# Kernel tuning notes

Measured on AMD Instinct MI355X. Metric: run time of the kernel, lower is better.

The kernel has to match this reference:

```python
import jax, jax.numpy as jnp
import numpy as np

NUM_HEADS = 8

def _ln(x, w, b, eps=1e-5):
    m = x.mean(-1, keepdims=True)
    v = ((x - m) ** 2).mean(-1, keepdims=True)
    return (x - m) / jnp.sqrt(v + eps) * w + b

def _l2n(x, axis=-1, eps=1e-12):
    n = jnp.linalg.norm(x, axis=axis, keepdims=True)
    return x / jnp.maximum(n, eps)

def setup_inputs() -> dict:
    key = jax.random.key(0)
    ks = jax.random.split(key, 30)
    B, N, C, nc, t = 2, 4096, 256, 150, 3
    Hh = Ww = 64
    hid = 4 * C
    s = 0.02
    inp = {}
    inp['x'] = jax.random.normal(ks[0], (B, N, C), jnp.float32)
    inp['z'] = jax.random.normal(ks[1], (B, nc, (t + 1) * N), jnp.float32)
    inp['mem'] = jax.random.normal(ks[2], (B * t, N, C), jnp.float32)
    inp['clustering_w'] = s * jax.random.normal(ks[3], (nc, C), jnp.float32)
    inp['prompt1'] = jax.random.normal(ks[4], (nc,), jnp.float32)
    inp['tdt1'] = jnp.eye(nc, dtype=jnp.float32) + s * jax.random.normal(ks[5], (nc, nc), jnp.float32)
    inp['prompt2'] = jax.random.normal(ks[6], (nc,), jnp.float32)
    inp['tdt2'] = jnp.eye(nc, dtype=jnp.float32) + s * jax.random.normal(ks[7], (nc, nc), jnp.float32)
    inp['sim_alpha'] = jnp.ones((1,), jnp.float32)
    inp['sim_beta'] = jnp.zeros((1,), jnp.float32)
    inp['q_w'] = s * jax.random.normal(ks[8], (C, C), jnp.float32)
    inp['q_b'] = s * jax.random.normal(ks[9], (C,), jnp.float32)
    inp['k_w'] = s * jax.random.normal(ks[10], (C, C), jnp.float32)
    inp['k_b'] = s * jax.random.normal(ks[11], (C,), jnp.float32)
    inp['v_w'] = s * jax.random.normal(ks[12], (C, C), jnp.float32)
    inp['v_b'] = s * jax.random.normal(ks[13], (C,), jnp.float32)
    inp['proj_w'] = s * jax.random.normal(ks[14], (C, C), jnp.float32)
    inp['proj_b'] = s * jax.random.normal(ks[15], (C,), jnp.float32)
    inp['norm_w'] = jnp.ones((C,), jnp.float32)
    inp['norm_b'] = jnp.zeros((C,), jnp.float32)
    inp['fc1_w'] = s * jax.random.normal(ks[16], (hid, C), jnp.float32)
    inp['fc1_b'] = s * jax.random.normal(ks[17], (hid,), jnp.float32)
    inp['dw_w'] = s * jax.random.normal(ks[18], (hid, 1, 3, 3), jnp.float32)
    inp['dw_b'] = s * jax.random.normal(ks[19], (hid,), jnp.float32)
    inp['fc2_w'] = s * jax.random.normal(ks[20], (C, hid), jnp.float32)
    inp['fc2_b'] = s * jax.random.normal(ks[21], (C,), jnp.float32)
    inp['H'] = Hh
    inp['W'] = Ww
    inp['t'] = t
    return inp

def _forward(x, z, mem, clustering_w, prompt1, tdt1, prompt2, tdt2, sim_alpha, sim_beta,
             q_w, q_b, k_w, k_b, v_w, v_b, proj_w, proj_b, norm_w, norm_b,
             fc1_w, fc1_b, dw_w, dw_b, fc2_w, fc2_b, H, W, t):
    B, N, C = x.shape
    nc = clustering_w.shape[0]
    res = x
    T = t + 1
    # cat memory frames with current frame: [(B*T), N, C]
    xf = jnp.concatenate([mem.reshape(B, t, N, C), x[:, None]], axis=1).reshape(B * T, N, C)
    # clustering head: (SRPS approximated as identity) 1x1 conv dim->num_clusters
    cl = jnp.einsum('bnc,kc->bkn', xf, clustering_w)            # [(B*T), nc, N]
    cl = cl.reshape(B, T, nc, N).transpose(0, 2, 1, 3).reshape(B, nc, T * N)
    # top-down prompt modulation of z and cluster logits
    zc = z.transpose(0, 2, 1)                                   # [B, T*N, nc]
    cos = _l2n(zc, -1) @ _l2n(prompt1[None, :, None], axis=1)   # [B, T*N, 1]
    zc = (zc * jnp.clip(cos, 0.0, 1.0)) @ tdt1
    clc = cl.transpose(0, 2, 1)
    cos = _l2n(clc, -1) @ _l2n(prompt2[None, :, None], axis=1)
    clc = (clc * jnp.clip(cos, 0.0, 1.0)) @ tdt2
    cluster_x_z = ((clc + zc) * 0.5).transpose(0, 2, 1)          # [B, nc, T*N]
    # inner_center: per-frame soft assignment -> cluster centers
    center = cluster_x_z.reshape(B, nc, T, N).transpose(0, 2, 1, 3)  # [B, T, nc, N]
    assigned_results = center
    soft = jax.nn.softmax(center, axis=-1)
    cx = xf.reshape(B, T, N, C)
    cen = jnp.einsum('btkn,btnc->btkc', soft, cx)               # [B, T, nc, C]
    last, prev = cen[:, -1], cen[:, :-1]                        # [B,nc,C], [B,t,nc,C]
    dot = jnp.einsum('bkc,btkc->btk', last, prev)
    denom = jnp.maximum(jnp.linalg.norm(last, axis=-1)[:, None] * jnp.linalg.norm(prev, axis=-1), 1e-8)
    gate = jax.nn.sigmoid(sim_beta + sim_alpha * (dot / denom))  # [B, t, nc]
    C_in = last + (gate[..., None] * prev).sum(axis=1)          # [B, nc, C]
    C_in = _ln(C_in, norm_w, norm_b)
    # cross attention: tokens query cluster centers
    hd = C // NUM_HEADS
    q = (res @ q_w.T + q_b) * (1.0 / np.sqrt(hd))
    k = C_in @ k_w.T + k_b
    v = C_in @ v_w.T + v_b
    q = q.reshape(B, N, NUM_HEADS, hd).transpose(0, 2, 1, 3)
    k = k.reshape(B, nc, NUM_HEADS, hd).transpose(0, 2, 1, 3)
    v = v.reshape(B, nc, NUM_HEADS, hd).transpose(0, 2, 1, 3)
    attn = jax.nn.softmax(jnp.einsum('bhnd,bhkd->bhnk', q, k), axis=-1)
    o = jnp.einsum('bhnk,bhkd->bhnd', attn, v).transpose(0, 2, 1, 3).reshape(B, N, C)
    o = o @ proj_w.T + proj_b
    out = res + _ln(o, norm_w, norm_b)
    # MLP with depthwise conv
    h = out @ fc1_w.T + fc1_b                                   # [B, N, 4C]
    hid = h.shape[-1]
    h_img = h.transpose(0, 2, 1).reshape(B, hid, H, W)
    h_img = jax.lax.conv_general_dilated(h_img, dw_w, (1, 1), 'SAME',
                                         feature_group_count=hid,
                                         dimension_numbers=('NCHW', 'OIHW', 'NCHW'))
    h_img = h_img + dw_b[None, :, None, None]
    h = h_img.reshape(B, hid, N).transpose(0, 2, 1)
    h = jax.nn.gelu(h, approximate=False) @ fc2_w.T + fc2_b
    out = out + _ln(h, norm_w, norm_b)
    return out, cluster_x_z, assigned_results

def reference(x, z, mem, clustering_w, prompt1, tdt1, prompt2, tdt2, sim_alpha, sim_beta,
              q_w, q_b, k_w, k_b, v_w, v_b, proj_w, proj_b, norm_w, norm_b,
              fc1_w, fc1_b, dw_w, dw_b, fc2_w, fc2_b, H, W, t):
    return _forward(x, z, mem, clustering_w, prompt1, tdt1, prompt2, tdt2, sim_alpha, sim_beta,
                    q_w, q_b, k_w, k_b, v_w, v_b, proj_w, proj_b, norm_w, norm_b,
                    fc1_w, fc1_b, dw_w, dw_b, fc2_w, fc2_b, H, W, t)
```

## Files before the change

kernel.cpp:

```cpp
#include <hip/hip_runtime.h>
#include <math.h>


typedef __attribute__((ext_vector_type(8))) short bf16x8;
typedef __attribute__((ext_vector_type(4))) float f32x4;

__device__ __forceinline__ short f2b(float f) {
  union { float f; unsigned int u; } c; c.f = f;
  unsigned int r = (c.u + 0x7fffu + ((c.u >> 16) & 1u)) >> 16;
  return (short)r;
}

__device__ __forceinline__ float bred_sum(float v, float* red) {
  int tid = threadIdx.x;
  red[tid] = v; __syncthreads();
  #pragma unroll
  for (int s = 128; s > 0; s >>= 1) {
    if (tid < s) red[tid] += red[tid + s];
    __syncthreads();
  }
  float r = red[0]; __syncthreads();
  return r;
}

__global__ __launch_bounds__(256) void gemm_mfma(
    const float* __restrict__ A, const float* __restrict__ W,
    const float* __restrict__ bias, float* __restrict__ out,
    int M, int N, int K, float alpha)
{
  __shared__ __align__(16) short As[64 * 72];
  __shared__ __align__(16) short Bs[64 * 72];
  const int tid = threadIdx.x;
  const int m0 = blockIdx.x * 64;
  const int n0 = blockIdx.y * 64;
  const int wave = tid >> 6;
  const int lane = tid & 63;
  const int wm = wave & 1, wn = wave >> 1;
  const int t16 = lane & 15;
  const int k8 = (lane >> 4) * 8;

  f32x4 acc[2][2];
  #pragma unroll
  for (int i = 0; i < 2; ++i)
    #pragma unroll
    for (int j = 0; j < 2; ++j)
      acc[i][j] = (f32x4){0.f, 0.f, 0.f, 0.f};

  const int sr = tid >> 2;
  const int sk = (tid & 3) * 16;

  for (int k0 = 0; k0 < K; k0 += 64) {
    {
      const float* ap = &A[(size_t)(m0 + sr) * K + k0 + sk];
      float4 v0 = *(const float4*)&ap[0];
      float4 v1 = *(const float4*)&ap[4];
      float4 v2 = *(const float4*)&ap[8];
      float4 v3 = *(const float4*)&ap[12];
      bf16x8 w0, w1;
      w0[0] = f2b(v0.x); w0[1] = f2b(v0.y); w0[2] = f2b(v0.z); w0[3] = f2b(v0.w);
      w0[4] = f2b(v1.x); w0[5] = f2b(v1.y); w0[6] = f2b(v1.z); w0[7] = f2b(v1.w);
      w1[0] = f2b(v2.x); w1[1] = f2b(v2.y); w1[2] = f2b(v2.z); w1[3] = f2b(v2.w);
      w1[4] = f2b(v3.x); w1[5] = f2b(v3.y); w1[6] = f2b(v3.z); w1[7] = f2b(v3.w);
      *(bf16x8*)&As[sr * 72 + sk] = w0;
      *(bf16x8*)&As[sr * 72 + sk + 8] = w1;
    }
    {
      const float* wp = &W[(size_t)(n0 + sr) * K + k0 + sk];
      float4 v0 = *(const float4*)&wp[0];
      float4 v1 = *(const float4*)&wp[4];
      float4 v2 = *(const float4*)&wp[8];
      float4 v3 = *(const float4*)&wp[12];
      bf16x8 w0, w1;
      w0[0] = f2b(v0.x); w0[1] = f2b(v0.y); w0[2] = f2b(v0.z); w0[3] = f2b(v0.w);
      w0[4] = f2b(v1.x); w0[5] = f2b(v1.y); w0[6] = f2b(v1.z); w0[7] = f2b(v1.w);
      w1[0] = f2b(v2.x); w1[1] = f2b(v2.y); w1[2] = f2b(v2.z); w1[3] = f2b(v2.w);
      w1[4] = f2b(v3.x); w1[5] = f2b(v3.y); w1[6] = f2b(v3.z); w1[7] = f2b(v3.w);
      *(bf16x8*)&Bs[sr * 72 + sk] = w0;
      *(bf16x8*)&Bs[sr * 72 + sk + 8] = w1;
    }
    __syncthreads();
    #pragma unroll
    for (int ks = 0; ks < 2; ++ks) {
      const int kofs = ks * 32 + k8;
      bf16x8 af0 = *(const bf16x8*)&As[(wm * 32 +  0 + t16) * 72 + kofs];
      bf16x8 af1 = *(const bf16x8*)&As[(wm * 32 + 16 + t16) * 72 + kofs];
      bf16x8 bf0 = *(const bf16x8*)&Bs[(wn * 32 +  0 + t16) * 72 + kofs];
      bf16x8 bf1 = *(const bf16x8*)&Bs[(wn * 32 + 16 + t16) * 72 + kofs];
      acc[0][0] = __builtin_amdgcn_mfma_f32_16x16x32_bf16(af0, bf0, acc[0][0], 0, 0, 0);
      acc[1][0] = __builtin_amdgcn_mfma_f32_16x16x32_bf16(af1, bf0, acc[1][0], 0, 0, 0);
      acc[0][1] = __builtin_amdgcn_mfma_f32_16x16x32_bf16(af0, bf1, acc[0][1], 0, 0, 0);
      acc[1][1] = __builtin_amdgcn_mfma_f32_16x16x32_bf16(af1, bf1, acc[1][1], 0, 0, 0);
    }
    __syncthreads();
  }
  const int r4 = (lane >> 4) * 4;
  #pragma unroll
  for (int ni = 0; ni < 2; ++ni) {
    const int gcol = n0 + wn * 32 + ni * 16 + t16;
    const float bb = bias[gcol];
    #pragma unroll
    for (int mi = 0; mi < 2; ++mi) {
      #pragma unroll
      for (int r = 0; r < 4; ++r) {
        const int gm = m0 + wm * 32 + mi * 16 + r4 + r;
        out[(size_t)gm * N + gcol] = alpha * (acc[mi][ni][r] + bb);
      }
    }
  }
}

__global__ __launch_bounds__(256) void prep_bt(
    const float* __restrict__ cw, const float* __restrict__ tdt2, const float* __restrict__ tdt1,
    short* __restrict__ cwb, short* __restrict__ TT)
{
  int idx = blockIdx.x * 256 + threadIdx.x;
  if (idx < 160 * 256) {
    int kc = idx >> 8, k = idx & 255;
    float v = (kc < 150) ? cw[kc * 256 + k] : 0.f;
    cwb[idx] = f2b(v);
  }
  if (idx < 160 * 320) {
    int kc = idx / 320, kk = idx - kc * 320;
    float t = 0.f;
    if (kc < 150) {
      if (kk < 150) t = tdt2[kk * 150 + kc];
      else if (kk >= 160 && kk < 310) t = tdt1[(kk - 160) * 150 + kc];
    }
    TT[idx] = f2b(t);
  }
}

__global__ __launch_bounds__(256) void xf_t(
    const float* __restrict__ x, const float* __restrict__ mem, short* __restrict__ xfT)
{
  __shared__ float tile[64][257];
  const int bt = blockIdx.y;
  const int n0 = blockIdx.x * 64;
  const int b = bt >> 2, ti = bt & 3;
  const float* xf = (ti < 3) ? (mem + (size_t)(b * 3 + ti) * 4096 * 256)
                             : (x + (size_t)b * 4096 * 256);
  const int tid = threadIdx.x;
  const int r = tid >> 2, cofs = (tid & 3) * 64;
  const float* src = xf + (size_t)(n0 + r) * 256 + cofs;
  #pragma unroll
  for (int i = 0; i < 16; ++i) {
    float4 v = *(const float4*)&src[i * 4];
    tile[r][cofs + i * 4 + 0] = v.x;
    tile[r][cofs + i * 4 + 1] = v.y;
    tile[r][cofs + i * 4 + 2] = v.z;
    tile[r][cofs + i * 4 + 3] = v.w;
  }
  __syncthreads();
  short* dst = xfT + ((size_t)bt * 256 + tid) * 4096 + n0;
  #pragma unroll
  for (int seg = 0; seg < 8; ++seg) {
    bf16x8 w;
    #pragma unroll
    for (int j = 0; j < 8; ++j) w[j] = f2b(tile[seg * 8 + j][tid]);
    *(bf16x8*)&dst[seg * 8] = w;
  }
}

__global__ __launch_bounds__(256) void fused_csz(
    const float* __restrict__ x, const float* __restrict__ mem, const float* __restrict__ z,
    const short* __restrict__ cwb, const short* __restrict__ TT,
    const float* __restrict__ p1, const float* __restrict__ p2,
    float* __restrict__ csz, float* __restrict__ asg)
{
  __shared__ __align__(16) short Acatile[64 * 328];
  __shared__ float p1s[160], p2s[160];
  __shared__ float sred[4][16][9];
  __shared__ float czs[64];
  const int tid = threadIdx.x;
  const int r0 = blockIdx.x * 64;
  const int b = r0 >> 14;
  const int mmg = r0 & 16383;
  const int ti = mmg >> 12, nn = mmg & 4095;
  const float* Ab = ((ti < 3) ? (mem + (size_t)(b * 3 + ti) * 4096 * 256)
                              : (x + (size_t)b * 4096 * 256)) + (size_t)nn * 256;
  const int wave = tid >> 6, lane = tid & 63;
  const int t16 = lane & 15, quad = lane >> 4, k8 = quad * 8;

  const int kr = tid >> 4, c4 = (tid & 15) * 4;
  float4 zv[10];
  #pragma unroll
  for (int it = 0; it < 10; ++it) {
    const int k = it * 16 + kr;
    zv[it] = make_float4(0.f, 0.f, 0.f, 0.f);
    if (k < 150) zv[it] = *(const float4*)&z[((size_t)b * 150 + k) * 16384 + mmg + c4];
  }
  if (tid < 160) {
    p2s[tid] = (tid < 150) ? p2[tid] : 0.f;
    p1s[tid] = (tid < 150) ? p1[tid] : 0.f;
  }

  f32x4 acc[10];
  #pragma unroll
  for (int i = 0; i < 10; ++i) acc[i] = (f32x4){0.f, 0.f, 0.f, 0.f};
  {
    const float* ap = Ab + (size_t)(wave * 16 + t16) * 256 + k8;
    const short* bp = cwb + t16 * 256 + k8;
    #pragma unroll 2
    for (int ks = 0; ks < 8; ++ks) {
      float4 v0 = *(const float4*)&ap[ks * 32];
      float4 v1 = *(const float4*)&ap[ks * 32 + 4];
      bf16x8 a;
      a[0] = f2b(v0.x); a[1] = f2b(v0.y); a[2] = f2b(v0.z); a[3] = f2b(v0.w);
      a[4] = f2b(v1.x); a[5] = f2b(v1.y); a[6] = f2b(v1.z); a[7] = f2b(v1.w);
      #pragma unroll
      for (int nf = 0; nf < 10; ++nf) {
        bf16x8 bv = *(const bf16x8*)&bp[nf * 4096 + ks * 32];
        acc[nf] = __builtin_amdgcn_mfma_f32_16x16x32_bf16(a, bv, acc[nf], 0, 0, 0);
      }
    }
  }
  __syncthreads();

  {
    float d[4] = {0.f, 0.f, 0.f, 0.f}, s[4] = {0.f, 0.f, 0.f, 0.f};
    float pn = 0.f;
    #pragma unroll
    for (int nf = 0; nf < 10; ++nf) {
      float a2 = p2s[nf * 16 + t16];
      pn += a2 * a2;
      #pragma unroll
      for (int r = 0; r < 4; ++r) {
        float v = acc[nf][r];
        d[r] = fmaf(v, a2, d[r]);
        s[r] = fmaf(v, v, s[r]);
      }
    }
    #pragma unroll
    for (int off = 1; off < 16; off <<= 1) {
      pn += __shfl_xor(pn, off);
      #pragma unroll
      for (int r = 0; r < 4; ++r) {
        d[r] += __shfl_xor(d[r], off);
        s[r] += __shfl_xor(s[r], off);
      }
    }
    const float spn = fmaxf(sqrtf(pn), 1e-12f);
    float cs[4];
    #pragma unroll
    for (int r = 0; r < 4; ++r) {
      float c = d[r] / (fmaxf(sqrtf(s[r]), 1e-12f) * spn);
      cs[r] = fminf(fmaxf(c, 0.f), 1.f);
    }
    #pragma unroll
    for (int nf = 0; nf < 10; ++nf)
      #pragma unroll
      for (int r = 0; r < 4; ++r)
        Acatile[(wave * 16 + quad * 4 + r) * 328 + nf * 16 + t16] = f2b(acc[nf][r] * cs[r]);
  }

  {
    float d[4] = {0.f, 0.f, 0.f, 0.f}, sv[4] = {0.f, 0.f, 0.f, 0.f};
    float pn = 0.f;
    #pragma unroll
    for (int it = 0; it < 10; ++it) {
      const int k = it * 16 + kr;
      const float a = p1s[k];
      d[0] = fmaf(zv[it].x, a, d[0]); d[1] = fmaf(zv[it].y, a, d[1]);
      d[2] = fmaf(zv[it].z, a, d[2]); d[3] = fmaf(zv[it].w, a, d[3]);
      sv[0] = fmaf(zv[it].x, zv[it].x, sv[0]); sv[1] = fmaf(zv[it].y, zv[it].y, sv[1]);
      sv[2] = fmaf(zv[it].z, zv[it].z, sv[2]); sv[3] = fmaf(zv[it].w, zv[it].w, sv[3]);
      pn = fmaf(a, a, pn);
    }
    #pragma unroll
    for (int off = 16; off < 64; off <<= 1) {
      pn += __shfl_xor(pn, off);
      #pragma unroll
      for (int r = 0; r < 4; ++r) {
        d[r] += __shfl_xor(d[r], off);
        sv[r] += __shfl_xor(sv[r], off);
      }
    }
    if ((lane >> 4) == 0) {
      #pragma unroll
      for (int r = 0; r < 4; ++r) {
        sred[wave][lane][r] = d[r];
        sred[wave][lane][4 + r] = sv[r];
      }
      sred[wave][lane][8] = pn;
    }
  }
  __syncthreads();
  if (tid < 64) {
    const int cg = tid >> 2, r = tid & 3;
    float dd = 0.f, ss = 0.f, pp = 0.f;
    #pragma unroll
    for (int w = 0; w < 4; ++w) {
      dd += sred[w][cg][r];
      ss += sred[w][cg][4 + r];
      pp += sred[w][cg][8];
    }
    float c = dd / (fmaxf(sqrtf(ss), 1e-12f) * fmaxf(sqrtf(pp), 1e-12f));
    czs[tid] = fminf(fmaxf(c, 0.f), 1.f);
  }
  __syncthreads();
  {
    const float cz0 = czs[c4 + 0], cz1 = czs[c4 + 1], cz2 = czs[c4 + 2], cz3 = czs[c4 + 3];
    #pragma unroll
    for (int it = 0; it < 10; ++it) {
      const int k = it * 16 + kr;
      Acatile[(c4 + 0) * 328 + 160 + k] = f2b(zv[it].x * cz0);
      Acatile[(c4 + 1) * 328 + 160 + k] = f2b(zv[it].y * cz1);
      Acatile[(c4 + 2) * 328 + 160 + k] = f2b(zv[it].z * cz2);
      Acatile[(c4 + 3) * 328 + 160 + k] = f2b(zv[it].w * cz3);
    }
  }
  __syncthreads();

  {
    const int wm = wave & 1, wn = wave >> 1;
    f32x4 c2[2][5];
    #pragma unroll
    for (int i = 0; i < 2; ++i)
      #pragma unroll
      for (int j = 0; j < 5; ++j)
        c2[i][j] = (f32x4){0.f, 0.f, 0.f, 0.f};
    const short* bp = TT + (size_t)(wn * 80 + t16) * 320 + k8;
    #pragma unroll 2
    for (int ks = 0; ks < 10; ++ks) {
      bf16x8 a0 = *(const bf16x8*)&Acatile[(wm * 32 + t16) * 328 + ks * 32 + k8];
      bf16x8 a1 = *(const bf16x8*)&Acatile[(wm * 32 + 16 + t16) * 328 + ks * 32 + k8];
      #pragma unroll
      for (int nf = 0; nf < 5; ++nf) {
        bf16x8 bv = *(const bf16x8*)&bp[nf * 5120 + ks * 32];
        c2[0][nf] = __builtin_amdgcn_mfma_f32_16x16x32_bf16(a0, bv, c2[0][nf], 0, 0, 0);
        c2[1][nf] = __builtin_amdgcn_mfma_f32_16x16x32_bf16(a1, bv, c2[1][nf], 0, 0, 0);
      }
    }
    #pragma unroll
    for (int nf = 0; nf < 5; ++nf) {
      const int kc = wn * 80 + nf * 16 + t16;
      if (kc < 150) {
        #pragma unroll
        for (int mf = 0; mf < 2; ++mf) {
          const int moff = wm * 32 + mf * 16 + quad * 4;
          float4 r4;
          r4.x = 0.5f * c2[mf][nf][0];
          r4.y = 0.5f * c2[mf][nf][1];
          r4.z = 0.5f * c2[mf][nf][2];
          r4.w = 0.5f * c2[mf][nf][3];
          *(float4*)&csz[((size_t)b * 150 + kc) * 16384 + mmg + moff] = r4;
          *(float4*)&asg[(((size_t)b * 4 + ti) * 150 + kc) * 4096 + nn + moff] = r4;
        }
      }
    }
  }
}

__global__ __launch_bounds__(256) void softmax_stats_e(
    const float* __restrict__ csz, float* __restrict__ lr_, short* __restrict__ ecsz)
{
  __shared__ float wred[8];
  const int row = blockIdx.x;
  const int bt = row / 150, k = row - bt * 150;
  const int b = bt >> 2, ti = bt & 3;
  const float* p = csz + ((size_t)b * 150 + k) * 16384 + ti * 4096;
  const int base = threadIdx.x * 16;
  float4 v[4];
  #pragma unroll
  for (int i = 0; i < 4; ++i) v[i] = *(const float4*)&p[base + i * 4];
  float mx = -1e30f;
  #pragma unroll
  for (int i = 0; i < 4; ++i)
    mx = fmaxf(mx, fmaxf(fmaxf(v[i].x, v[i].y), fmaxf(v[i].z, v[i].w)));
  #pragma unroll
  for (int off = 1; off < 64; off <<= 1) mx = fmaxf(mx, __shfl_xor(mx, off));
  const int wave = threadIdx.x >> 6, lane = threadIdx.x & 63;
  if (lane == 0) wred[wave] = mx;
  __syncthreads();
  mx = fmaxf(fmaxf(wred[0], wred[1]), fmaxf(wred[2], wred[3]));
  const float L = 1.4426950408889634f;
  float s = 0.f;
  bf16x8 e0, e1;
  #pragma unroll
  for (int i = 0; i < 2; ++i) {
    float a = exp2f((v[i].x - mx) * L);
    float bq = exp2f((v[i].y - mx) * L);
    float cq = exp2f((v[i].z - mx) * L);
    float dq = exp2f((v[i].w - mx) * L);
    s += a + bq + cq + dq;
    e0[i * 4 + 0] = f2b(a); e0[i * 4 + 1] = f2b(bq); e0[i * 4 + 2] = f2b(cq); e0[i * 4 + 3] = f2b(dq);
  }
  #pragma unroll
  for (int i = 2; i < 4; ++i) {
    float a = exp2f((v[i].x - mx) * L);
    float bq = exp2f((v[i].y - mx) * L);
    float cq = exp2f((v[i].z - mx) * L);
    float dq = exp2f((v[i].w - mx) * L);
    s += a + bq + cq + dq;
    e1[(i - 2) * 4 + 0] = f2b(a); e1[(i - 2) * 4 + 1] = f2b(bq);
    e1[(i - 2) * 4 + 2] = f2b(cq); e1[(i - 2) * 4 + 3] = f2b(dq);
  }
  #pragma unroll
  for (int off = 1; off < 64; off <<= 1) s += __shfl_xor(s, off);
  if (lane == 0) wred[4 + wave] = s;
  __syncthreads();
  short* er = ecsz + ((size_t)bt * 160 + k) * 4096 + base;
  *(bf16x8*)&er[0] = e0;
  *(bf16x8*)&er[8] = e1;
  if (threadIdx.x == 0) lr_[row] = wred[4] + wred[5] + wred[6] + wred[7];
}

__global__ __launch_bounds__(256) void gemm_cen_at(
    const short* __restrict__ ecsz, const short* __restrict__ xfT,
    float* __restrict__ cen)
{
  __shared__ __align__(16) short As[160 * 136];
  const int tid = threadIdx.x;
  const int chalf = blockIdx.x;
  const int bt = blockIdx.y;
  const int sp = blockIdx.z;
  const int n0 = sp * 128;
  const int wave = tid >> 6, lane = tid & 63;
  const int t16 = lane & 15, quad = lane >> 4, k8 = quad * 8;
  const int cbase = chalf * 128 + wave * 32;

  f32x4 acc[10][2];
  #pragma unroll
  for (int i = 0; i < 10; ++i) {
    acc[i][0] = (f32x4){0.f, 0.f, 0.f, 0.f};
    acc[i][1] = (f32x4){0.f, 0.f, 0.f, 0.f};
  }

  const short* erow = ecsz + (size_t)bt * 160 * 4096 + n0;
  #pragma unroll
  for (int p = 0; p < 10; ++p) {
    const int g = p * 256 + tid;
    const int row = g >> 4;
    const int col8 = (g & 15) * 8;
    *(bf16x8*)&As[row * 136 + col8] = *(const bf16x8*)&erow[(size_t)row * 4096 + col8];
  }
  __syncthreads();
  const short* xrow = xfT + (size_t)bt * 256 * 4096 + n0;
  #pragma unroll
  for (int kc = 0; kc < 4; ++kc) {
    bf16x8 b0 = *(const bf16x8*)&xrow[(size_t)(cbase + t16) * 4096 + kc * 32 + k8];
    bf16x8 b1 = *(const bf16x8*)&xrow[(size_t)(cbase + 16 + t16) * 4096 + kc * 32 + k8];
    #pragma unroll
    for (int mt = 0; mt < 10; ++mt) {
      bf16x8 aA = *(const bf16x8*)&As[(mt * 16 + t16) * 136 + kc * 32 + k8];
      acc[mt][0] = __builtin_amdgcn_mfma_f32_16x16x32_bf16(aA, b0, acc[mt][0], 0, 0, 0);
      acc[mt][1] = __builtin_amdgcn_mfma_f32_16x16x32_bf16(aA, b1, acc[mt][1], 0, 0, 0);
    }
  }
  #pragma unroll
  for (int mt = 0; mt < 10; ++mt) {
    #pragma unroll
    for (int r = 0; r < 4; ++r) {
      const int grow = mt * 16 + quad * 4 + r;
      if (grow < 150) {
        atomicAdd(&cen[((size_t)bt * 150 + grow) * 256 + cbase + t16], acc[mt][0][r]);
        atomicAdd(&cen[((size_t)bt * 150 + grow) * 256 + cbase + 16 + t16], acc[mt][1][r]);
      }
    }
  }
}

__global__ __launch_bounds__(256) void gate_ln(
    const float* __restrict__ cen, const float* __restrict__ lr_,
    const float* __restrict__ alpha_, const float* __restrict__ beta_,
    const float* __restrict__ nw, const float* __restrict__ nb, float* __restrict__ cin)
{
  __shared__ float red[256];
  int bk = blockIdx.x;
  int b = bk / 150, k = bk % 150;
  int c = threadIdx.x;
  const float* base = cen + ((size_t)b * 4 * 150) * 256;
  const float* lrb = lr_ + (size_t)b * 4 * 150;
  float lc  = base[((size_t)3 * 150 + k) * 256 + c] / lrb[3 * 150 + k];
  float p0  = base[((size_t)0 * 150 + k) * 256 + c] / lrb[0 * 150 + k];
  float p1v = base[((size_t)1 * 150 + k) * 256 + c] / lrb[1 * 150 + k];
  float p2v = base[((size_t)2 * 150 + k) * 256 + c] / lrb[2 * 150 + k];
  float nl = bred_sum(lc * lc, red);
  float q0 = bred_sum(p0 * p0, red);
  float q1 = bred_sum(p1v * p1v, red);
  float q2 = bred_sum(p2v * p2v, red);
  float d0 = bred_sum(lc * p0, red);
  float d1 = bred_sum(lc * p1v, red);
  float d2 = bred_sum(lc * p2v, red);
  float al = alpha_[0], be = beta_[0];
  float snl = sqrtf(nl);
  float g0 = 1.f / (1.f + expf(-(be + al * (d0 / fmaxf(snl * sqrtf(q0), 1e-8f)))));
  float g1 = 1.f / (1.f + expf(-(be + al * (d1 / fmaxf(snl * sqrtf(q1), 1e-8f)))));
  float g2 = 1.f / (1.f + expf(-(be + al * (d2 / fmaxf(snl * sqrtf(q2), 1e-8f)))));
  float ci = lc + g0 * p0 + g1 * p1v + g2 * p2v;
  float mu = bred_sum(ci, red) * (1.f / 256.f);
  float df = ci - mu;
  float var = bred_sum(df * df, red) * (1.f / 256.f);
  cin[(size_t)bk * 256 + c] = df * rsqrtf(var + 1e-5f) * nw[c] + nb[c];
}

__global__ __launch_bounds__(256) void gemm_nt(
    const float* __restrict__ A, const float* __restrict__ W,
    const float* __restrict__ bias, float* __restrict__ out,
    int M, int N, int K, float alpha)
{
  __shared__ __align__(16) float As[16][132];
  __shared__ __align__(16) float Ws[16][68];
  const int tid = threadIdx.x;
  const int m0 = blockIdx.x * 128;
  const int n0 = blockIdx.y * 64;
  const int tm = tid & 15;
  const int tn = tid >> 4;
  float acc[8][4];
  #pragma unroll
  for (int i = 0; i < 8; ++i)
    #pragma unroll
    for (int j = 0; j < 4; ++j) acc[i][j] = 0.f;

  const int lr = tid >> 2;
  const int lk = (tid & 3) * 4;

  for (int k0 = 0; k0 < K; k0 += 16) {
    #pragma unroll
    for (int p = 0; p < 2; ++p) {
      int r = lr + p * 64;
      int gm = m0 + r;
      float4 v = make_float4(0.f, 0.f, 0.f, 0.f);
      if (gm < M) v = *(const float4*)&A[(size_t)gm * K + k0 + lk];
      As[lk + 0][r] = v.x; As[lk + 1][r] = v.y; As[lk + 2][r] = v.z; As[lk + 3][r] = v.w;
    }
    {
      float4 v = *(const float4*)&W[(size_t)(n0 + lr) * K + k0 + lk];
      Ws[lk + 0][lr] = v.x; Ws[lk + 1][lr] = v.y; Ws[lk + 2][lr] = v.z; Ws[lk + 3][lr] = v.w;
    }
    __syncthreads();
    #pragma unroll
    for (int kk = 0; kk < 16; ++kk) {
      float4 a0 = *(const float4*)&As[kk][tm * 8];
      float4 a1 = *(const float4*)&As[kk][tm * 8 + 4];
      float4 w0 = *(const float4*)&Ws[kk][tn * 4];
      float av[8] = {a0.x, a0.y, a0.z, a0.w, a1.x, a1.y, a1.z, a1.w};
      float wv[4] = {w0.x, w0.y, w0.z, w0.w};
      #pragma unroll
      for (int i = 0; i < 8; ++i)
        #pragma unroll
        for (int j = 0; j < 4; ++j)
          acc[i][j] = fmaf(av[i], wv[j], acc[i][j]);
    }
    __syncthreads();
  }
  float4 bv = *(const float4*)&bias[n0 + tn * 4];
  float bb[4] = {bv.x, bv.y, bv.z, bv.w};
  #pragma unroll
  for (int i = 0; i < 8; ++i) {
    int gm = m0 + tm * 8 + i;
    if (gm >= M) continue;
    float4 r;
    r.x = alpha * (acc[i][0] + bb[0]);
    r.y = alpha * (acc[i][1] + bb[1]);
    r.z = alpha * (acc[i][2] + bb[2]);
    r.w = alpha * (acc[i][3] + bb[3]);
    *(float4*)&out[(size_t)gm * N + n0 + tn * 4] = r;
  }
}

__global__ __launch_bounds__(256) void attn_mfma(
    const float* __restrict__ q, const float* __restrict__ ks, const float* __restrict__ vs,
    float* __restrict__ o)
{
  __shared__ __align__(16) short Ps[128 * 168];
  __shared__ __align__(16) short VT[32 * 168];
  __shared__ float lrow[128];
  const int tid = threadIdx.x;
  const int bid = blockIdx.x;
  const int ntile = bid & 31;
  const int bh = bid >> 5;
  const int b = bh >> 3, h = bh & 7;
  const int n0 = ntile * 128;
  const int wave = tid >> 6, lane = tid & 63;
  const int t16 = lane & 15, quad = lane >> 4;
  const int k8 = quad * 8;
  const int wr = wave * 32;

  for (int i = tid; i < 5120; i += 256) {
    int d = i / 160, kc = i - d * 160;
    VT[d * 168 + kc] = (kc < 150) ? f2b(vs[((size_t)b * 150 + kc) * 256 + h * 32 + d]) : (short)0;
  }

  bf16x8 aQ[2];
  #pragma unroll
  for (int mt = 0; mt < 2; ++mt) {
    const float* qp = &q[((size_t)b * 4096 + n0 + wr + mt * 16 + t16) * 256 + h * 32 + k8];
    float4 v0 = *(const float4*)&qp[0];
    float4 v1 = *(const float4*)&qp[4];
    bf16x8 w;
    w[0] = f2b(v0.x); w[1] = f2b(v0.y); w[2] = f2b(v0.z); w[3] = f2b(v0.w);
    w[4] = f2b(v1.x); w[5] = f2b(v1.y); w[6] = f2b(v1.z); w[7] = f2b(v1.w);
    aQ[mt] = w;
  }

  f32x4 s[2][10];
  #pragma unroll
  for (int ct = 0; ct < 10; ++ct) {
    const int c = ct * 16 + t16;
    bf16x8 bK = {0, 0, 0, 0, 0, 0, 0, 0};
    if (c < 150) {
      const float* kp = &ks[((size_t)b * 150 + c) * 256 + h * 32 + k8];
      float4 v0 = *(const float4*)&kp[0];
      float4 v1 = *(const float4*)&kp[4];
      bK[0] = f2b(v0.x); bK[1] = f2b(v0.y); bK[2] = f2b(v0.z); bK[3] = f2b(v0.w);
      bK[4] = f2b(v1.x); bK[5] = f2b(v1.y); bK[6] = f2b(v1.z); bK[7] = f2b(v1.w);
    }
    f32x4 zero = (f32x4){0.f, 0.f, 0.f, 0.f};
    s[0][ct] = __builtin_amdgcn_mfma_f32_16x16x32_bf16(aQ[0], bK, zero, 0, 0, 0);
    s[1][ct] = __builtin_amdgcn_mfma_f32_16x16x32_bf16(aQ[1], bK, zero, 0, 0, 0);
  }

  #pragma unroll
  for (int mt = 0; mt < 2; ++mt) {
    #pragma unroll
    for (int r = 0; r < 4; ++r) {
      float mx = -1e30f;
      #pragma unroll
      for (int ct = 0; ct < 10; ++ct) {
        float v = s[mt][ct][r];
        if (ct == 9 && t16 >= 6) { v = -1e30f; s[mt][ct][r] = v; }
        mx = fmaxf(mx, v);
      }
      mx = fmaxf(mx, __shfl_xor(mx, 1));
      mx = fmaxf(mx, __shfl_xor(mx, 2));
      mx = fmaxf(mx, __shfl_xor(mx, 4));
      mx = fmaxf(mx, __shfl_xor(mx, 8));
      float ls = 0.f;
      #pragma unroll
      for (int ct = 0; ct < 10; ++ct) {
        float e = expf(s[mt][ct][r] - mx);
        s[mt][ct][r] = e;
        ls += e;
      }
      ls += __shfl_xor(ls, 1);
      ls += __shfl_xor(ls, 2);
      ls += __shfl_xor(ls, 4);
      ls += __shfl_xor(ls, 8);
      if (t16 == 0) lrow[wr + mt * 16 + quad * 4 + r] = 1.f / ls;
      #pragma unroll
      for (int ct = 0; ct < 10; ++ct)
        Ps[(wr + mt * 16 + quad * 4 + r) * 168 + ct * 16 + t16] = f2b(s[mt][ct][r]);
    }
  }
  __syncthreads();

  f32x4 oacc[2][2];
  #pragma unroll
  for (int i = 0; i < 2; ++i)
    #pragma unroll
    for (int j = 0; j < 2; ++j)
      oacc[i][j] = (f32x4){0.f, 0.f, 0.f, 0.f};
  #pragma unroll
  for (int kstep = 0; kstep < 5; ++kstep) {
    bf16x8 bV0 = *(const bf16x8*)&VT[( 0 + t16) * 168 + kstep * 32 + k8];
    bf16x8 bV1 = *(const bf16x8*)&VT[(16 + t16) * 168 + kstep * 32 + k8];
    #pragma unroll
    for (int mt = 0; mt < 2; ++mt) {
      bf16x8 aP = *(const bf16x8*)&Ps[(wr + mt * 16 + t16) * 168 + kstep * 32 + k8];
      oacc[mt][0] = __builtin_amdgcn_mfma_f32_16x16x32_bf16(aP, bV0, oacc[mt][0], 0, 0, 0);
      oacc[mt][1] = __builtin_amdgcn_mfma_f32_16x16x32_bf16(aP, bV1, oacc[mt][1], 0, 0, 0);
    }
  }
  #pragma unroll
  for (int mt = 0; mt < 2; ++mt) {
    #pragma unroll
    for (int nt = 0; nt < 2; ++nt) {
      const int d = nt * 16 + t16;
      #pragma unroll
      for (int r = 0; r < 4; ++r) {
        const int row = wr + mt * 16 + quad * 4 + r;
        o[((size_t)b * 4096 + n0 + row) * 256 + h * 32 + d] = oacc[mt][nt][r] * lrow[row];
      }
    }
  }
}

__global__ __launch_bounds__(256) void ln_res(
    const float* __restrict__ src, const float* __restrict__ res,
    const float* __restrict__ nw, const float* __restrict__ nb, float* __restrict__ dst)
{
  const int wave = threadIdx.x >> 6;
  const int lane = threadIdx.x & 63;
  const size_t row = (size_t)blockIdx.x * 4 + wave;
  const int c = lane * 4;
  float4 v = *(const float4*)&src[row * 256 + c];
  float s  = v.x + v.y + v.z + v.w;
  float s2 = v.x * v.x + v.y * v.y + v.z * v.z + v.w * v.w;
  #pragma unroll
  for (int off = 1; off < 64; off <<= 1) {
    s  += __shfl_xor(s, off);
    s2 += __shfl_xor(s2, off);
  }
  const float mu = s * (1.f / 256.f);
  const float var = s2 * (1.f / 256.f) - mu * mu;
  const float inv = rsqrtf(var + 1e-5f);
  float4 w = *(const float4*)&nw[c];
  float4 bb = *(const float4*)&nb[c];
  float4 rr = *(const float4*)&res[row * 256 + c];
  float4 d;
  d.x = rr.x + (v.x - mu) * inv * w.x + bb.x;
  d.y = rr.y + (v.y - mu) * inv * w.y + bb.y;
  d.z = rr.z + (v.z - mu) * inv * w.z + bb.z;
  d.w = rr.w + (v.w - mu) * inv * w.w + bb.w;
  *(float4*)&dst[row * 256 + c] = d;
}

__global__ __launch_bounds__(256) void conv_wt(
    const float* __restrict__ w, float* __restrict__ wt)
{
  int i = blockIdx.x * 256 + threadIdx.x;
  if (i < 9216) {
    int ch = i / 9, tap = i - ch * 9;
    wt[tap * 1024 + ch] = w[i];
  }
}

__global__ __launch_bounds__(256) void conv_gelu(
    const float* __restrict__ h, const float* __restrict__ wt, const float* __restrict__ bias,
    float* __restrict__ hc)
{
  const int bid = blockIdx.x;
  const int xg = bid & 15;
  const int y  = (bid >> 4) & 63;
  const int b  = bid >> 10;
  const int x0 = xg * 4;
  const int c4 = threadIdx.x * 4;
  const float* hb = h + ((size_t)b * 4096) * 1024 + c4;

  float4 tap[3][6];
  #pragma unroll
  for (int dy = 0; dy < 3; ++dy) {
    const int yy = y + dy - 1;
    #pragma unroll
    for (int dx = 0; dx < 6; ++dx) {
      const int xv = x0 + dx - 1;
      tap[dy][dx] = make_float4(0.f, 0.f, 0.f, 0.f);
      if (yy >= 0 && yy <= 63 && xv >= 0 && xv <= 63)
        tap[dy][dx] = *(const float4*)&hb[(size_t)(yy * 64 + xv) * 1024];
    }
  }
  float4 wv[3][3];
  #pragma unroll
  for (int dy = 0; dy < 3; ++dy)
    #pragma unroll
    for (int dx = 0; dx < 3; ++dx)
      wv[dy][dx] = *(const float4*)&wt[(dy * 3 + dx) * 1024 + c4];
  const float4 bv = *(const float4*)&bias[c4];

  #pragma unroll
  for (int p = 0; p < 4; ++p) {
    float4 acc = bv;
    #pragma unroll
    for (int dy = 0; dy < 3; ++dy) {
      #pragma unroll
      for (int dx = 0; dx < 3; ++dx) {
        const float4 hv = tap[dy][p + dx];
        const float4 w = wv[dy][dx];
        acc.x = fmaf(hv.x, w.x, acc.x);
        acc.y = fmaf(hv.y, w.y, acc.y);
        acc.z = fmaf(hv.z, w.z, acc.z);
        acc.w = fmaf(hv.w, w.w, acc.w);
      }
    }
    float4 g;
    g.x = 0.5f * acc.x * (1.f + erff(acc.x * 0.70710678118654752f));
    g.y = 0.5f * acc.y * (1.f + erff(acc.y * 0.70710678118654752f));
    g.z = 0.5f * acc.z * (1.f + erff(acc.z * 0.70710678118654752f));
    g.w = 0.5f * acc.w * (1.f + erff(acc.w * 0.70710678118654752f));
    *(float4*)&hc[((size_t)b * 4096 + y * 64 + x0 + p) * 1024 + c4] = g;
  }
}

extern "C" void kernel_launch(void* const* d_in, const int* in_sizes, int n_in,
                              void* d_out, int out_size, void* d_ws, size_t ws_size,
                              hipStream_t stream)
{
  (void)in_sizes; (void)n_in; (void)out_size; (void)ws_size;
  const float* x    = (const float*)d_in[0];
  const float* z    = (const float*)d_in[1];
  const float* mem  = (const float*)d_in[2];
  const float* cw   = (const float*)d_in[3];
  const float* p1   = (const float*)d_in[4];
  const float* tdt1 = (const float*)d_in[5];
  const float* p2   = (const float*)d_in[6];
  const float* tdt2 = (const float*)d_in[7];
  const float* sal  = (const float*)d_in[8];
  const float* sbe  = (const float*)d_in[9];
  const float* q_w  = (const float*)d_in[10];
  const float* q_b  = (const float*)d_in[11];
  const float* k_w  = (const float*)d_in[12];
  const float* k_b  = (const float*)d_in[13];
  const float* v_w  = (const float*)d_in[14];
  const float* v_b  = (const float*)d_in[15];
  const float* pj_w = (const float*)d_in[16];
  const float* pj_b = (const float*)d_in[17];
  const float* nw   = (const float*)d_in[18];
  const float* nb   = (const float*)d_in[19];
  const float* f1w  = (const float*)d_in[20];
  const float* f1b  = (const float*)d_in[21];
  const float* dww  = (const float*)d_in[22];
  const float* dwb  = (const float*)d_in[23];
  const float* f2w  = (const float*)d_in[24];
  const float* f2b_ = (const float*)d_in[25];

  float* out = (float*)d_out;
  float* csz = out + 2097152;
  float* asg = csz + 4915200;

  float* ws    = (float*)d_ws;
  short* ecsz  = (short*)ws;
  short* TT    = (short*)(ws + 5242880);
  short* cwb   = (short*)(ws + 5275648);
  float* lr_   = ws + 5308416;
  float* cen   = ws + 5310816;
  float* cin   = ws + 5618016;
  float* q     = ws + 5694816;
  float* ksb   = ws + 7791968;
  float* vsb   = ws + 7868768;
  float* o     = ws + 7945568;
  short* xfT   = (short*)(ws + 10042720);
  float* h     = ws;
  float* hc    = ws + 8388608;
  float* tmp   = ws + 16777216;
  float* out1  = ws + 18874368;
  float* wt    = ws + 20971520;

  dim3 blk(256);
  prep_bt<<<dim3(200), blk, 0, stream>>>(cw, tdt2, tdt1, cwb, TT);
  xf_t<<<dim3(64, 8), blk, 0, stream>>>(x, mem, xfT);
  fused_csz<<<dim3(512), blk, 0, stream>>>(x, mem, z, cwb, TT, p1, p2, csz, asg);
  softmax_stats_e<<<dim3(1200), blk, 0, stream>>>(csz, lr_, ecsz);
  hipMemsetAsync(cen, 0, (size_t)1200 * 256 * sizeof(float), stream);
  gemm_cen_at<<<dim3(2, 8, 32), blk, 0, stream>>>(ecsz, xfT, cen);
  gate_ln<<<dim3(300), blk, 0, stream>>>(cen, lr_, sal, sbe, nw, nb, cin);
  gemm_mfma<<<dim3(128, 4), blk, 0, stream>>>(x, q_w, q_b, q, 8192, 256, 256, 0.17677669529663687f);
  gemm_nt<<<dim3(3, 4), blk, 0, stream>>>(cin, k_w, k_b, ksb, 300, 256, 256, 1.f);
  gemm_nt<<<dim3(3, 4), blk, 0, stream>>>(cin, v_w, v_b, vsb, 300, 256, 256, 1.f);
  attn_mfma<<<dim3(512), blk, 0, stream>>>(q, ksb, vsb, o);
  gemm_mfma<<<dim3(128, 4), blk, 0, stream>>>(o, pj_w, pj_b, tmp, 8192, 256, 256, 1.f);
  ln_res<<<dim3(2048), blk, 0, stream>>>(tmp, x, nw, nb, out1);
  gemm_mfma<<<dim3(128, 16), blk, 0, stream>>>(out1, f1w, f1b, h, 8192, 1024, 256, 1.f);
  conv_wt<<<dim3(36), blk, 0, stream>>>(dww, wt);
  conv_gelu<<<dim3(2048), blk, 0, stream>>>(h, wt, dwb, hc);
  gemm_mfma<<<dim3(128, 4), blk, 0, stream>>>(hc, f2w, f2b_, tmp, 8192, 256, 1024, 1.f);
  ln_res<<<dim3(2048), blk, 0, stream>>>(tmp, out1, nw, nb, out);
}
```

Before: 422.6 us.

## Fuse output-projection and fc2 GEMMs with LayerNorm residual epilogue

Adds a GEMM kernel where each block computes a 16-row by 256-column tile, so every block holds complete rows and can apply bias, LayerNorm and the residual add in its epilogue. This replaces the proj and fc2 gemm_mfma launches and their separate ln_res passes, removing the intermediate tmp buffer write and re-read plus two launches. The cost is that each 16-row block reloads and converts the entire weight matrix to bf16 per k-step, which means much more weight traffic and lower reuse than the previous 64x64 tiling.

```diff
diff --git a/kernel.cpp b/kernel.cpp
--- a/kernel.cpp
+++ b/kernel.cpp
@@ -3,6 +3,7 @@
 
 
 typedef __attribute__((ext_vector_type(8))) short bf16x8;
+typedef __attribute__((ext_vector_type(4))) short bf16x4;
 typedef __attribute__((ext_vector_type(4))) float f32x4;
 
 __device__ __forceinline__ short f2b(float f) {
@@ -105,6 +106,117 @@
         const int gm = m0 + wm * 32 + mi * 16 + r4 + r;
         out[(size_t)gm * N + gcol] = alpha * (acc[mi][ni][r] + bb);
       }
+    }
+  }
+}
+
+__global__ __launch_bounds__(256) void gemm_ln_res(
+    const float* __restrict__ A, const float* __restrict__ W,
+    const float* __restrict__ bias, const float* __restrict__ res,
+    const float* __restrict__ nw, const float* __restrict__ nb,
+    float* __restrict__ dst, int K)
+{
+  __shared__ __align__(16) short As[16 * 72];
+  __shared__ __align__(16) short Bs[256 * 72];
+  __shared__ float red[16][4][2];
+  const int tid = threadIdx.x;
+  const int m0 = blockIdx.x * 16;
+  const int wave = tid >> 6, lane = tid & 63;
+  const int t16 = lane & 15, quad = lane >> 4, k8 = quad * 8;
+
+  f32x4 acc[4];
+  #pragma unroll
+  for (int i = 0; i < 4; ++i) acc[i] = (f32x4){0.f, 0.f, 0.f, 0.f};
+
+  const int sr = tid >> 2;
+  const int sk = (tid & 3) * 16;
+  const int arow = tid >> 4, akc = (tid & 15) * 4;
+
+  for (int k0 = 0; k0 < K; k0 += 64) {
+    {
+      float4 v = *(const float4*)&A[(size_t)(m0 + arow) * K + k0 + akc];
+      bf16x4 w;
+      w[0] = f2b(v.x); w[1] = f2b(v.y); w[2] = f2b(v.z); w[3] = f2b(v.w);
+      *(bf16x4*)&As[arow * 72 + akc] = w;
+    }
+    #pragma unroll
+    for (int p = 0; p < 4; ++p) {
+      const float* wp = &W[(size_t)(p * 64 + sr) * K + k0 + sk];
+      float4 v0 = *(const float4*)&wp[0];
+      float4 v1 = *(const float4*)&wp[4];
+      float4 v2 = *(const float4*)&wp[8];
+      float4 v3 = *(const float4*)&wp[12];
+      bf16x8 w0, w1;
+      w0[0] = f2b(v0.x); w0[1] = f2b(v0.y); w0[2] = f2b(v0.z); w0[3] = f2b(v0.w);
+      w0[4] = f2b(v1.x); w0[5] = f2b(v1.y); w0[6] = f2b(v1.z); w0[7] = f2b(v1.w);
+      w1[0] = f2b(v2.x); w1[1] = f2b(v2.y); w1[2] = f2b(v2.z); w1[3] = f2b(v2.w);
+      w1[4] = f2b(v3.x); w1[5] = f2b(v3.y); w1[6] = f2b(v3.z); w1[7] = f2b(v3.w);
+      *(bf16x8*)&Bs[(p * 64 + sr) * 72 + sk] = w0;
+      *(bf16x8*)&Bs[(p * 64 + sr) * 72 + sk + 8] = w1;
+    }
+    __syncthreads();
+    #pragma unroll
+    for (int ks = 0; ks < 2; ++ks) {
+      const int kofs = ks * 32 + k8;
+      bf16x8 af = *(const bf16x8*)&As[t16 * 72 + kofs];
+      #pragma unroll
+      for (int ni = 0; ni < 4; ++ni) {
+        bf16x8 bf = *(const bf16x8*)&Bs[(wave * 64 + ni * 16 + t16) * 72 + kofs];
+        acc[ni] = __builtin_amdgcn_mfma_f32_16x16x32_bf16(af, bf, acc[ni], 0, 0, 0);
+      }
+    }
+    __syncthreads();
+  }
+
+  const int gcolb = wave * 64;
+  float val[4][4];
+  float s[4] = {0.f, 0.f, 0.f, 0.f}, s2[4] = {0.f, 0.f, 0.f, 0.f};
+  #pragma unroll
+  for (int ni = 0; ni < 4; ++ni) {
+    const float bb = bias[gcolb + ni * 16 + t16];
+    #pragma unroll
+    for (int r = 0; r < 4; ++r) {
+      float v = acc[ni][r] + bb;
+      val[ni][r] = v;
+      s[r] += v;
+      s2[r] = fmaf(v, v, s2[r]);
+    }
+  }
+  #pragma unroll
+  for (int off = 1; off < 16; off <<= 1) {
+    #pragma unroll
+    for (int r = 0; r < 4; ++r) {
+      s[r] += __shfl_xor(s[r], off);
+      s2[r] += __shfl_xor(s2[r], off);
+    }
+  }
+  if (t16 == 0) {
+    #pragma unroll
+    for (int r = 0; r < 4; ++r) {
+      red[quad * 4 + r][wave][0] = s[r];
+      red[quad * 4 + r][wave][1] = s2[r];
+    }
+  }
+  __syncthreads();
+  float mu[4], inv[4];
+  #pragma unroll
+  for (int r = 0; r < 4; ++r) {
+    const int row = quad * 4 + r;
+    float st  = red[row][0][0] + red[row][1][0] + red[row][2][0] + red[row][3][0];
+    float st2 = red[row][0][1] + red[row][1][1] + red[row][2][1] + red[row][3][1];
+    float m = st * (1.f / 256.f);
+    mu[r] = m;
+    inv[r] = rsqrtf(st2 * (1.f / 256.f) - m * m + 1e-5f);
+  }
+  #pragma unroll
+  for (int ni = 0; ni < 4; ++ni) {
+    const int gcol = gcolb + ni * 16 + t16;
+    const float wc = nw[gcol], bc = nb[gcol];
+    #pragma unroll
+    for (int r = 0; r < 4; ++r) {
+      const int gm = m0 + quad * 4 + r;
+      dst[(size_t)gm * 256 + gcol] =
+          res[(size_t)gm * 256 + gcol] + (val[ni][r] - mu[r]) * inv[r] * wc + bc;
     }
   }
 }
@@ -676,36 +788,6 @@
   }
 }
 
-__global__ __launch_bounds__(256) void ln_res(
-    const float* __restrict__ src, const float* __restrict__ res,
-    const float* __restrict__ nw, const float* __restrict__ nb, float* __restrict__ dst)
-{
-  const int wave = threadIdx.x >> 6;
-  const int lane = threadIdx.x & 63;
-  const size_t row = (size_t)blockIdx.x * 4 + wave;
-  const int c = lane * 4;
-  float4 v = *(const float4*)&src[row * 256 + c];
-  float s  = v.x + v.y + v.z + v.w;
-  float s2 = v.x * v.x + v.y * v.y + v.z * v.z + v.w * v.w;
-  #pragma unroll
-  for (int off = 1; off < 64; off <<= 1) {
-    s  += __shfl_xor(s, off);
-    s2 += __shfl_xor(s2, off);
-  }
-  const float mu = s * (1.f / 256.f);
-  const float var = s2 * (1.f / 256.f) - mu * mu;
-  const float inv = rsqrtf(var + 1e-5f);
-  float4 w = *(const float4*)&nw[c];
-  float4 bb = *(const float4*)&nb[c];
-  float4 rr = *(const float4*)&res[row * 256 + c];
-  float4 d;
-  d.x = rr.x + (v.x - mu) * inv * w.x + bb.x;
-  d.y = rr.y + (v.y - mu) * inv * w.y + bb.y;
-  d.z = rr.z + (v.z - mu) * inv * w.z + bb.z;
-  d.w = rr.w + (v.w - mu) * inv * w.w + bb.w;
-  *(float4*)&dst[row * 256 + c] = d;
-}
-
 __global__ __launch_bounds__(256) void conv_wt(
     const float* __restrict__ w, float* __restrict__ wt)
 {
@@ -822,7 +904,6 @@
   short* xfT   = (short*)(ws + 10042720);
   float* h     = ws;
   float* hc    = ws + 8388608;
-  float* tmp   = ws + 16777216;
   float* out1  = ws + 18874368;
   float* wt    = ws + 20971520;
 
@@ -838,11 +919,9 @@
   gemm_nt<<<dim3(3, 4), blk, 0, stream>>>(cin, k_w, k_b, ksb, 300, 256, 256, 1.f);
   gemm_nt<<<dim3(3, 4), blk, 0, stream>>>(cin, v_w, v_b, vsb, 300, 256, 256, 1.f);
   attn_mfma<<<dim3(512), blk, 0, stream>>>(q, ksb, vsb, o);
-  gemm_mfma<<<dim3(128, 4), blk, 0, stream>>>(o, pj_w, pj_b, tmp, 8192, 256, 256, 1.f);
-  ln_res<<<dim3(2048), blk, 0, stream>>>(tmp, x, nw, nb, out1);
+  gemm_ln_res<<<dim3(512), blk, 0, stream>>>(o, pj_w, pj_b, x, nw, nb, out1, 256);
   gemm_mfma<<<dim3(128, 16), blk, 0, stream>>>(out1, f1w, f1b, h, 8192, 1024, 256, 1.f);
   conv_wt<<<dim3(36), blk, 0, stream>>>(dww, wt);
   conv_gelu<<<dim3(2048), blk, 0, stream>>>(h, wt, dwb, hc);
-  gemm_mfma<<<dim3(128, 4), blk, 0, stream>>>(hc, f2w, f2b_, tmp, 8192, 256, 1024, 1.f);
-  ln_res<<<dim3(2048), blk, 0, stream>>>(tmp, out1, nw, nb, out);
-}
+  gemm_ln_res<<<dim3(512), blk, 0, stream>>>(hc, f2w, f2b_, out1, nw, nb, out, 1024);
+}
```

Measured after the change: 453.5 us. 1.07x slower.
